# Kernel tuning notes

Measured on AMD Instinct MI355X. Metric: run time of the kernel, lower is better.

The kernel has to match this reference:

```python
import jax, jax.numpy as jnp
import numpy as np

B = 4096   # batch
I = 1024   # in_features
O = 1024   # out_features
N = 4      # LUT fan-in; table size 2**N = 16


def setup_inputs() -> dict:
    key = jax.random.key(0)
    k1, k2, k3 = jax.random.split(key, 3)
    return {
        "x": jax.random.normal(k1, (B, I), dtype=jnp.float32),
        # learnable mapping logits: (out_features, n, in_features)
        "mapping_logits": jax.random.normal(k2, (O, N, I), dtype=jnp.float32),
        # per-node LUT tables with 2**n corner values each
        "lut_tables": jax.random.normal(k3, (O, 2 ** N), dtype=jnp.float32),
    }


def reference(x, mapping_logits, lut_tables):
    # softmax-weighted input selection: (B,I) x (O,N,I) -> (B,O,N)
    w = jax.nn.softmax(mapping_logits, axis=-1)
    selected = jnp.einsum('bi,oni->bon', x, w)
    # BatchedLUTNodes: squash to [0,1], multilinear interpolation over 2**N corners
    s = jax.nn.sigmoid(selected)                      # (B,O,N)
    cw = jnp.ones(s.shape[:2] + (1,), dtype=s.dtype)  # corner weights, grows to (B,O,2**N)
    for j in range(N):                                # fixed small loop over fan-in
        sj = s[..., j][..., None]                     # (B,O,1)
        cw = jnp.concatenate([cw * (1.0 - sj), cw * sj], axis=-1)
    # weighted sum of per-node table entries -> (B,O)
    return jnp.einsum('boc,oc->bo', cw, lut_tables)
```

## Files before the change

kernel.cpp:

```cpp
#include <hip/hip_runtime.h>

#define B_DIM 4096
#define I_DIM 1024
#define O_DIM 1024
#define ON_DIM 4096
#define TILE_HALFS 4096

typedef _Float16 half8  __attribute__((ext_vector_type(8)));
typedef _Float16 half4_t __attribute__((ext_vector_type(4)));
typedef float    floatx4 __attribute__((ext_vector_type(4)));

__global__ __launch_bounds__(256)
void ltn_prep(const float* __restrict__ logits, const float* __restrict__ x,
              _Float16* __restrict__ wt, _Float16* __restrict__ xt) {
  __shared__ _Float16 tile[TILE_HALFS];
  const int t = threadIdx.x, lane = t & 63, wv = t >> 6;
  if (blockIdx.x < 1024) {
    const int row = blockIdx.x * 4 + wv;
    const float4* src = (const float4*)(logits + (size_t)row * I_DIM);
    float4 v[4];
#pragma unroll
    for (int j = 0; j < 4; j++) v[j] = src[j * 64 + lane];
    float m = -1e30f;
#pragma unroll
    for (int j = 0; j < 4; j++)
      m = fmaxf(m, fmaxf(fmaxf(v[j].x, v[j].y), fmaxf(v[j].z, v[j].w)));
#pragma unroll
    for (int off = 1; off < 64; off <<= 1) m = fmaxf(m, __shfl_xor(m, off));
    float e[16];
    float s = 0.0f;
#pragma unroll
    for (int j = 0; j < 4; j++) {
      e[4 * j + 0] = __expf(v[j].x - m);
      e[4 * j + 1] = __expf(v[j].y - m);
      e[4 * j + 2] = __expf(v[j].z - m);
      e[4 * j + 3] = __expf(v[j].w - m);
      s += (e[4 * j + 0] + e[4 * j + 1]) + (e[4 * j + 2] + e[4 * j + 3]);
    }
#pragma unroll
    for (int off = 1; off < 64; off <<= 1) s += __shfl_xor(s, off);
    const float inv = 1.0f / s;
    const int nb = row >> 7, nn = row & 127;
    _Float16* base = wt + (size_t)nb * 32 * TILE_HALFS + nn * 8;
#pragma unroll
    for (int jj = 0; jj < 4; jj++) {
      const int k0g  = jj * 256 + lane * 4;
      const int kb32 = k0g >> 5;
      const int kb8  = (k0g >> 3) & 3;
      const int jr   = k0g & 7;
      half4_t h;
      h[0] = (_Float16)(e[4 * jj + 0] * inv);
      h[1] = (_Float16)(e[4 * jj + 1] * inv);
      h[2] = (_Float16)(e[4 * jj + 2] * inv);
      h[3] = (_Float16)(e[4 * jj + 3] * inv);
      *(half4_t*)(base + (size_t)kb32 * TILE_HALFS + kb8 * 1024 + jr) = h;
    }
  } else {
    const int bid = blockIdx.x - 1024;
    const int mb = bid & 31, kt = bid >> 5;
    const int r8 = t >> 3, c4 = (t & 7) * 4;
    const int kb8 = c4 >> 3, jr = c4 & 7;
#pragma unroll
    for (int p = 0; p < 4; p++) {
      const int row = p * 32 + r8;
      const float4 v = *(const float4*)(
          x + (size_t)(mb * 128 + row) * I_DIM + kt * 32 + c4);
      half4_t h;
      h[0] = (_Float16)v.x; h[1] = (_Float16)v.y;
      h[2] = (_Float16)v.z; h[3] = (_Float16)v.w;
      *(half4_t*)&tile[kb8 * 1024 + row * 8 + jr] = h;
    }
    __syncthreads();
    _Float16* dst = xt + (size_t)(mb * 32 + kt) * TILE_HALFS;
    ((half8*)dst)[t]       = ((const half8*)tile)[t];
    ((half8*)dst)[256 + t] = ((const half8*)tile)[256 + t];
  }
}

__global__ __launch_bounds__(256)
void ltn_gemm_lut(const _Float16* __restrict__ xt,
                  const _Float16* __restrict__ wt,
                  const float* __restrict__ lut,
                  float* __restrict__ out) {
  __shared__ _Float16 As[4][128][8];
  __shared__ _Float16 Bs[4][128][8];

  const int tid  = threadIdx.x;
  const int lane = tid & 63;
  const int wv   = tid >> 6;
  const int wr   = wv >> 1;
  const int wc   = wv & 1;
  const int mb   = blockIdx.x;
  const int nb   = blockIdx.y;
  const int bm0  = mb * 128;
  const int bn0  = nb * 128;
  const int fm   = lane & 15;
  const int kq   = lane >> 4;

  floatx4 acc[4][4];
#pragma unroll
  for (int i = 0; i < 4; i++)
#pragma unroll
    for (int j = 0; j < 4; j++) acc[i][j] = (floatx4)0.0f;

  for (int kt = 0; kt < 32; kt++) {
    const _Float16* tA = xt + (size_t)(mb * 32 + kt) * TILE_HALFS;
    const _Float16* tB = wt + (size_t)(nb * 32 + kt) * TILE_HALFS;
#pragma unroll
    for (int s = 0; s < 2; s++) {
      const int c = wv * 2 + s;
      const _Float16* gA = tA + c * 512 + lane * 8;
      const _Float16* gB = tB + c * 512 + lane * 8;
      __builtin_amdgcn_global_load_lds(
          (const __attribute__((address_space(1))) void*)gA,
          (__attribute__((address_space(3))) void*)((char*)&As[0][0][0] + c * 1024),
          16, 0, 0);
      __builtin_amdgcn_global_load_lds(
          (const __attribute__((address_space(1))) void*)gB,
          (__attribute__((address_space(3))) void*)((char*)&Bs[0][0][0] + c * 1024),
          16, 0, 0);
    }
    __syncthreads();

    half8 af[4], bf[4];
#pragma unroll
    for (int f = 0; f < 4; f++) {
      af[f] = *(const half8*)&As[kq][wr * 64 + f * 16 + fm][0];
      bf[f] = *(const half8*)&Bs[kq][wc * 64 + f * 16 + fm][0];
    }
#pragma unroll
    for (int mt = 0; mt < 4; mt++)
#pragma unroll
      for (int nt = 0; nt < 4; nt++)
        acc[mt][nt] = __builtin_amdgcn_mfma_f32_16x16x32_f16(
            af[mt], bf[nt], acc[mt][nt], 0, 0, 0);
    __syncthreads();
  }

#pragma unroll
  for (int nt = 0; nt < 4; nt++) {
    const int o = (bn0 + wc * 64 + nt * 16 + (lane & 15)) >> 2;
    const float4* lt4 = (const float4*)(lut + (size_t)o * 16);
    const float4 L0 = lt4[0], L1 = lt4[1], L2 = lt4[2], L3 = lt4[3];
#pragma unroll
    for (int mt = 0; mt < 4; mt++) {
#pragma unroll
      for (int r = 0; r < 4; r++) {
        const float v  = acc[mt][nt][r];
        const float sv = 1.0f / (1.0f + __expf(-v));
        const float s1 = __shfl_down(sv, 1);
        const float s2 = __shfl_down(sv, 2);
        const float s3 = __shfl_down(sv, 3);
        if ((lane & 3) == 0) {
          const float s0 = sv;
          const float a0 = L0.x + (L2.x - L0.x) * s3;
          const float a1 = L0.y + (L2.y - L0.y) * s3;
          const float a2 = L0.z + (L2.z - L0.z) * s3;
          const float a3 = L0.w + (L2.w - L0.w) * s3;
          const float a4 = L1.x + (L3.x - L1.x) * s3;
          const float a5 = L1.y + (L3.y - L1.y) * s3;
          const float a6 = L1.z + (L3.z - L1.z) * s3;
          const float a7 = L1.w + (L3.w - L1.w) * s3;
          const float b0 = a0 + (a4 - a0) * s2;
          const float b1 = a1 + (a5 - a1) * s2;
          const float b2 = a2 + (a6 - a2) * s2;
          const float b3 = a3 + (a7 - a3) * s2;
          const float c0 = b0 + (b2 - b0) * s1;
          const float c1 = b1 + (b3 - b1) * s1;
          const float res = c0 + (c1 - c0) * s0;
          const int row = bm0 + wr * 64 + mt * 16 + (lane >> 4) * 4 + r;
          out[(size_t)row * O_DIM + o] = res;
        }
      }
    }
  }
}

extern "C" void kernel_launch(void* const* d_in, const int* in_sizes, int n_in,
                              void* d_out, int out_size, void* d_ws, size_t ws_size,
                              hipStream_t stream) {
  const float* x      = (const float*)d_in[0];
  const float* logits = (const float*)d_in[1];
  const float* lut    = (const float*)d_in[2];
  float* out          = (float*)d_out;

  _Float16* wt = (_Float16*)d_ws;
  _Float16* xt = (_Float16*)d_ws + (size_t)ON_DIM * I_DIM;

  ltn_prep<<<2048, 256, 0, stream>>>(logits, x, wt, xt);
  dim3 grid(B_DIM / 128, ON_DIM / 128);
  ltn_gemm_lut<<<grid, 256, 0, stream>>>(xt, wt, lut, out);
}
```

Baseline: 142.9 us.

## Enlarge GEMM tile to 256x256 with double-buffered LDS and split prep kernels

The GEMM now uses 512-thread blocks computing 256x256 output tiles, with each wave holding a 4x8 MFMA accumulator grid. Its LDS buffers are double-buffered so the next k-tile's global-to-LDS load overlaps the current MFMA work, with one barrier per iteration. The prep stage is split into a softmax-statistics kernel and a tiling kernel that writes half8 vectors straight to global memory, dropping the LDS transpose. This costs an extra launch, recomputes the exponentials, uses the output buffer as scratch for the stats, and raises register pressure (32 accumulators per wave), which may limit occupancy.

Result: faster. 133.7 us (-6.5%).

```diff
diff --git a/kernel.cpp b/kernel.cpp
--- a/kernel.cpp
+++ b/kernel.cpp
@@ -11,79 +11,87 @@
 typedef float    floatx4 __attribute__((ext_vector_type(4)));
 
 __global__ __launch_bounds__(256)
-void ltn_prep(const float* __restrict__ logits, const float* __restrict__ x,
+void ltn_stats(const float* __restrict__ logits, float2* __restrict__ stats) {
+  const int t = threadIdx.x, lane = t & 63, wv = t >> 6;
+  const int row = blockIdx.x * 4 + wv;
+  const float4* src = (const float4*)(logits + (size_t)row * I_DIM);
+  float4 v[4];
+#pragma unroll
+  for (int j = 0; j < 4; j++) v[j] = src[j * 64 + lane];
+  float m = -1e30f;
+#pragma unroll
+  for (int j = 0; j < 4; j++)
+    m = fmaxf(m, fmaxf(fmaxf(v[j].x, v[j].y), fmaxf(v[j].z, v[j].w)));
+#pragma unroll
+  for (int off = 1; off < 64; off <<= 1) m = fmaxf(m, __shfl_xor(m, off));
+  float s = 0.0f;
+#pragma unroll
+  for (int j = 0; j < 4; j++) {
+    s += __expf(v[j].x - m) + __expf(v[j].y - m)
+       + __expf(v[j].z - m) + __expf(v[j].w - m);
+  }
+#pragma unroll
+  for (int off = 1; off < 64; off <<= 1) s += __shfl_xor(s, off);
+  if (lane == 0) stats[row] = make_float2(m, 1.0f / s);
+}
+
+__global__ __launch_bounds__(256)
+void ltn_tile(const float* __restrict__ logits, const float* __restrict__ x,
+              const float2* __restrict__ stats,
               _Float16* __restrict__ wt, _Float16* __restrict__ xt) {
-  __shared__ _Float16 tile[TILE_HALFS];
-  const int t = threadIdx.x, lane = t & 63, wv = t >> 6;
+  const int t  = threadIdx.x;
+  const int nn = t >> 1;
+  const int hf = t & 1;
   if (blockIdx.x < 1024) {
-    const int row = blockIdx.x * 4 + wv;
-    const float4* src = (const float4*)(logits + (size_t)row * I_DIM);
-    float4 v[4];
-#pragma unroll
-    for (int j = 0; j < 4; j++) v[j] = src[j * 64 + lane];
-    float m = -1e30f;
-#pragma unroll
-    for (int j = 0; j < 4; j++)
-      m = fmaxf(m, fmaxf(fmaxf(v[j].x, v[j].y), fmaxf(v[j].z, v[j].w)));
-#pragma unroll
-    for (int off = 1; off < 64; off <<= 1) m = fmaxf(m, __shfl_xor(m, off));
-    float e[16];
-    float s = 0.0f;
-#pragma unroll
-    for (int j = 0; j < 4; j++) {
-      e[4 * j + 0] = __expf(v[j].x - m);
-      e[4 * j + 1] = __expf(v[j].y - m);
-      e[4 * j + 2] = __expf(v[j].z - m);
-      e[4 * j + 3] = __expf(v[j].w - m);
-      s += (e[4 * j + 0] + e[4 * j + 1]) + (e[4 * j + 2] + e[4 * j + 3]);
-    }
-#pragma unroll
-    for (int off = 1; off < 64; off <<= 1) s += __shfl_xor(s, off);
-    const float inv = 1.0f / s;
-    const int nb = row >> 7, nn = row & 127;
-    _Float16* base = wt + (size_t)nb * 32 * TILE_HALFS + nn * 8;
-#pragma unroll
-    for (int jj = 0; jj < 4; jj++) {
-      const int k0g  = jj * 256 + lane * 4;
-      const int kb32 = k0g >> 5;
-      const int kb8  = (k0g >> 3) & 3;
-      const int jr   = k0g & 7;
-      half4_t h;
-      h[0] = (_Float16)(e[4 * jj + 0] * inv);
-      h[1] = (_Float16)(e[4 * jj + 1] * inv);
-      h[2] = (_Float16)(e[4 * jj + 2] * inv);
-      h[3] = (_Float16)(e[4 * jj + 3] * inv);
-      *(half4_t*)(base + (size_t)kb32 * TILE_HALFS + kb8 * 1024 + jr) = h;
-    }
+    const int nb = blockIdx.x >> 5, kb = blockIdx.x & 31;
+    const int row = nb * 128 + nn;
+    const float2 st = stats[row];
+    const float4* src = (const float4*)(logits + (size_t)row * I_DIM + kb * 32 + hf * 16);
+    const float4 a = src[0], b = src[1], c = src[2], d = src[3];
+    half8 h0, h1;
+    h0[0] = (_Float16)(__expf(a.x - st.x) * st.y);
+    h0[1] = (_Float16)(__expf(a.y - st.x) * st.y);
+    h0[2] = (_Float16)(__expf(a.z - st.x) * st.y);
+    h0[3] = (_Float16)(__expf(a.w - st.x) * st.y);
+    h0[4] = (_Float16)(__expf(b.x - st.x) * st.y);
+    h0[5] = (_Float16)(__expf(b.y - st.x) * st.y);
+    h0[6] = (_Float16)(__expf(b.z - st.x) * st.y);
+    h0[7] = (_Float16)(__expf(b.w - st.x) * st.y);
+    h1[0] = (_Float16)(__expf(c.x - st.x) * st.y);
+    h1[1] = (_Float16)(__expf(c.y - st.x) * st.y);
+    h1[2] = (_Float16)(__expf(c.z - st.x) * st.y);
+    h1[3] = (_Float16)(__expf(c.w - st.x) * st.y);
+    h1[4] = (_Float16)(__expf(d.x - st.x) * st.y);
+    h1[5] = (_Float16)(__expf(d.y - st.x) * st.y);
+    h1[6] = (_Float16)(__expf(d.z - st.x) * st.y);
+    h1[7] = (_Float16)(__expf(d.w - st.x) * st.y);
+    _Float16* base = wt + ((size_t)nb * 32 + kb) * TILE_HALFS + (hf * 2) * 1024 + nn * 8;
+    *(half8*)base = h0;
+    *(half8*)(base + 1024) = h1;
   } else {
     const int bid = blockIdx.x - 1024;
-    const int mb = bid & 31, kt = bid >> 5;
-    const int r8 = t >> 3, c4 = (t & 7) * 4;
-    const int kb8 = c4 >> 3, jr = c4 & 7;
-#pragma unroll
-    for (int p = 0; p < 4; p++) {
-      const int row = p * 32 + r8;
-      const float4 v = *(const float4*)(
-          x + (size_t)(mb * 128 + row) * I_DIM + kt * 32 + c4);
-      half4_t h;
-      h[0] = (_Float16)v.x; h[1] = (_Float16)v.y;
-      h[2] = (_Float16)v.z; h[3] = (_Float16)v.w;
-      *(half4_t*)&tile[kb8 * 1024 + row * 8 + jr] = h;
-    }
-    __syncthreads();
-    _Float16* dst = xt + (size_t)(mb * 32 + kt) * TILE_HALFS;
-    ((half8*)dst)[t]       = ((const half8*)tile)[t];
-    ((half8*)dst)[256 + t] = ((const half8*)tile)[256 + t];
-  }
-}
-
-__global__ __launch_bounds__(256)
+    const int mb = bid >> 5, kt = bid & 31;
+    const int row = mb * 128 + nn;
+    const float4* src = (const float4*)(x + (size_t)row * I_DIM + kt * 32 + hf * 16);
+    const float4 a = src[0], b = src[1], c = src[2], d = src[3];
+    half8 h0, h1;
+    h0[0] = (_Float16)a.x; h0[1] = (_Float16)a.y; h0[2] = (_Float16)a.z; h0[3] = (_Float16)a.w;
+    h0[4] = (_Float16)b.x; h0[5] = (_Float16)b.y; h0[6] = (_Float16)b.z; h0[7] = (_Float16)b.w;
+    h1[0] = (_Float16)c.x; h1[1] = (_Float16)c.y; h1[2] = (_Float16)c.z; h1[3] = (_Float16)c.w;
+    h1[4] = (_Float16)d.x; h1[5] = (_Float16)d.y; h1[6] = (_Float16)d.z; h1[7] = (_Float16)d.w;
+    _Float16* base = xt + ((size_t)mb * 32 + kt) * TILE_HALFS + (hf * 2) * 1024 + nn * 8;
+    *(half8*)base = h0;
+    *(half8*)(base + 1024) = h1;
+  }
+}
+
+__global__ __launch_bounds__(512, 2)
 void ltn_gemm_lut(const _Float16* __restrict__ xt,
                   const _Float16* __restrict__ wt,
                   const float* __restrict__ lut,
                   float* __restrict__ out) {
-  __shared__ _Float16 As[4][128][8];
-  __shared__ _Float16 Bs[4][128][8];
+  __shared__ _Float16 As[2][2][4][128][8];
+  __shared__ _Float16 Bs[2][2][4][128][8];
 
   const int tid  = threadIdx.x;
   const int lane = tid & 63;
@@ -92,54 +100,68 @@
   const int wc   = wv & 1;
   const int mb   = blockIdx.x;
   const int nb   = blockIdx.y;
-  const int bm0  = mb * 128;
-  const int bn0  = nb * 128;
   const int fm   = lane & 15;
   const int kq   = lane >> 4;
 
-  floatx4 acc[4][4];
+  const size_t baseA = (size_t)(mb * 2) * 32 * TILE_HALFS;
+  const size_t baseB = (size_t)(nb * 2) * 32 * TILE_HALFS;
+
+  floatx4 acc[4][8];
 #pragma unroll
   for (int i = 0; i < 4; i++)
 #pragma unroll
-    for (int j = 0; j < 4; j++) acc[i][j] = (floatx4)0.0f;
-
-  for (int kt = 0; kt < 32; kt++) {
-    const _Float16* tA = xt + (size_t)(mb * 32 + kt) * TILE_HALFS;
-    const _Float16* tB = wt + (size_t)(nb * 32 + kt) * TILE_HALFS;
-#pragma unroll
-    for (int s = 0; s < 2; s++) {
-      const int c = wv * 2 + s;
-      const _Float16* gA = tA + c * 512 + lane * 8;
-      const _Float16* gB = tB + c * 512 + lane * 8;
+    for (int j = 0; j < 8; j++) acc[i][j] = (floatx4)0.0f;
+
+  auto stage = [&](int buf, int kt) {
+#pragma unroll
+    for (int s = 0; s < 4; s++) {
+      const int c   = wv * 4 + s;
+      const int cc  = c & 15;
+      const int tl  = cc >> 3;
+      const int sub = cc & 7;
+      const _Float16* g;
+      char* l;
+      if (c < 16) {
+        g = xt + baseA + (size_t)(tl * 32 + kt) * TILE_HALFS + sub * 512 + lane * 8;
+        l = (char*)&As[buf][0][0][0][0] + cc * 1024;
+      } else {
+        g = wt + baseB + (size_t)(tl * 32 + kt) * TILE_HALFS + sub * 512 + lane * 8;
+        l = (char*)&Bs[buf][0][0][0][0] + cc * 1024;
+      }
       __builtin_amdgcn_global_load_lds(
-          (const __attribute__((address_space(1))) void*)gA,
-          (__attribute__((address_space(3))) void*)((char*)&As[0][0][0] + c * 1024),
-          16, 0, 0);
-      __builtin_amdgcn_global_load_lds(
-          (const __attribute__((address_space(1))) void*)gB,
-          (__attribute__((address_space(3))) void*)((char*)&Bs[0][0][0] + c * 1024),
-          16, 0, 0);
+          (const __attribute__((address_space(1))) void*)g,
+          (__attribute__((address_space(3))) void*)l, 16, 0, 0);
     }
-    __syncthreads();
-
-    half8 af[4], bf[4];
-#pragma unroll
-    for (int f = 0; f < 4; f++) {
-      af[f] = *(const half8*)&As[kq][wr * 64 + f * 16 + fm][0];
-      bf[f] = *(const half8*)&Bs[kq][wc * 64 + f * 16 + fm][0];
-    }
+  };
+
+  auto compute = [&](int buf) {
+    half8 af[4], bf[8];
+#pragma unroll
+    for (int f = 0; f < 4; f++)
+      af[f] = *(const half8*)&As[buf][wr >> 1][kq][(wr & 1) * 64 + f * 16 + fm][0];
+#pragma unroll
+    for (int g = 0; g < 8; g++)
+      bf[g] = *(const half8*)&Bs[buf][wc][kq][g * 16 + fm][0];
 #pragma unroll
     for (int mt = 0; mt < 4; mt++)
 #pragma unroll
-      for (int nt = 0; nt < 4; nt++)
+      for (int nt = 0; nt < 8; nt++)
         acc[mt][nt] = __builtin_amdgcn_mfma_f32_16x16x32_f16(
             af[mt], bf[nt], acc[mt][nt], 0, 0, 0);
+  };
+
+  stage(0, 0);
+  int buf = 0;
+  for (int kt = 0; kt < 32; kt++) {
     __syncthreads();
-  }
-
-#pragma unroll
-  for (int nt = 0; nt < 4; nt++) {
-    const int o = (bn0 + wc * 64 + nt * 16 + (lane & 15)) >> 2;
+    if (kt + 1 < 32) stage(buf ^ 1, kt + 1);
+    compute(buf);
+    buf ^= 1;
+  }
+
+#pragma unroll
+  for (int nt = 0; nt < 8; nt++) {
+    const int o = (nb * 256 + wc * 128 + nt * 16 + fm) >> 2;
     const float4* lt4 = (const float4*)(lut + (size_t)o * 16);
     const float4 L0 = lt4[0], L1 = lt4[1], L2 = lt4[2], L3 = lt4[3];
 #pragma unroll
@@ -168,7 +190,7 @@
           const float c0 = b0 + (b2 - b0) * s1;
           const float c1 = b1 + (b3 - b1) * s1;
           const float res = c0 + (c1 - c0) * s0;
-          const int row = bm0 + wr * 64 + mt * 16 + (lane >> 4) * 4 + r;
+          const int row = mb * 256 + wr * 64 + mt * 16 + (lane >> 4) * 4 + r;
           out[(size_t)row * O_DIM + o] = res;
         }
       }
@@ -186,8 +208,10 @@
 
   _Float16* wt = (_Float16*)d_ws;
   _Float16* xt = (_Float16*)d_ws + (size_t)ON_DIM * I_DIM;
-
-  ltn_prep<<<2048, 256, 0, stream>>>(logits, x, wt, xt);
-  dim3 grid(B_DIM / 128, ON_DIM / 128);
-  ltn_gemm_lut<<<grid, 256, 0, stream>>>(xt, wt, lut, out);
-}
+  float2* stats = (float2*)d_out;
+
+  ltn_stats<<<1024, 256, 0, stream>>>(logits, stats);
+  ltn_tile<<<2048, 256, 0, stream>>>(logits, x, stats, wt, xt);
+  dim3 grid(16, 16);
+  ltn_gemm_lut<<<grid, 512, 0, stream>>>(xt, wt, lut, out);
+}
```
